# Kernel optimization log

Hardware: AMD Instinct MI355X
Metric: run time of the kernel (lower is better)

The kernel has to match this reference:

```python
import jax, jax.numpy as jnp
import numpy as np

N_NODES = 50000
N_EDGES = 800000
N_RELS = 16
D = 128


def _rgcn_layer(h, W, b, loop_w, gate_w, src, dst, rel, norm, apply_relu, n_nodes):
    # Transform all node features by every relation weight once: [R, N, D_out].
    # Equivalent to DGL bmm_maybe_select's per-edge W[rel] bmm, but avoids an
    # [E, D, D] gather of weights.
    h_all = jnp.einsum('nd,rde->rne', h, W)
    msg = h_all[rel, src]                                    # [E, D_out]
    msg = msg * norm                                         # edge norm scaling
    gate_logit = jnp.einsum('nd,rd->rn', h, gate_w[..., 0])  # [R, N]
    gate = jax.nn.sigmoid(gate_logit[rel, src])[:, None]     # [E, 1]
    msg = msg * gate
    agg = jax.ops.segment_sum(msg, dst, num_segments=n_nodes)  # fn.sum -> dst
    out = agg + b + h @ loop_w                               # bias + self loop
    if apply_relu:
        out = jax.nn.relu(out)
    return out  # dropout is identity in eval mode


def setup_inputs() -> dict:
    key = jax.random.key(0)
    ks = jax.random.split(key, 12)
    gain = float(np.sqrt(2.0))  # relu gain (xavier-ish scale; values arbitrary)
    def xav(k, shape):
        fan = shape[-2] + shape[-1]
        s = gain * np.sqrt(6.0 / fan)
        return jax.random.uniform(k, shape, jnp.float32, -s, s)
    return {
        'h': jax.random.normal(ks[0], (N_NODES, D), jnp.float32),
        'norm': jax.random.uniform(ks[1], (N_EDGES, 1), jnp.float32),
        'weight0': xav(ks[2], (N_RELS, D, D)),
        'bias0': jnp.zeros((D,), jnp.float32),
        'loop_w0': xav(ks[3], (D, D)),
        'gate_w0': xav(ks[4], (N_RELS, D, 1)),
        'weight1': xav(ks[5], (N_RELS, D, D)),
        'bias1': jnp.zeros((D,), jnp.float32),
        'loop_w1': xav(ks[6], (D, D)),
        'gate_w1': xav(ks[7], (N_RELS, D, 1)),
        'src': jax.random.randint(ks[8], (N_EDGES,), 0, N_NODES, jnp.int32),
        'dst': jax.random.randint(ks[9], (N_EDGES,), 0, N_NODES, jnp.int32),
        'rel_type': jax.random.randint(ks[10], (N_EDGES,), 0, N_RELS, jnp.int32),
    }


def reference(h, norm, weight0, bias0, loop_w0, gate_w0,
              weight1, bias1, loop_w1, gate_w1, src, dst, rel_type):
    n_nodes = h.shape[0]
    # Layer 0: activation=relu (idx < num_hidden_layers - 1)
    h = _rgcn_layer(h, weight0, bias0, loop_w0, gate_w0, src, dst, rel_type,
                    norm, True, n_nodes)
    # Layer 1: no activation
    h = _rgcn_layer(h, weight1, bias1, loop_w1, gate_w1, src, dst, rel_type,
                    norm, False, n_nodes)
    return h
```

## Files before the change

kernel.cpp:

```cpp
#include <hip/hip_runtime.h>
#include <hip/hip_bf16.h>
#include <stdint.h>

#define NN 50000
#define NE 800000
#define NR 16
#define NP (NN * NR)
#define NB1 ((NP + 255) / 256)
#define NTILES ((NN + 127) / 128)

typedef unsigned short u16;
typedef unsigned int u32;

typedef __bf16 bf16x8 __attribute__((ext_vector_type(8)));
typedef __bf16 bf16x2 __attribute__((ext_vector_type(2)));
typedef float f32x4 __attribute__((ext_vector_type(4)));

__device__ __forceinline__ u16 f2bf(float f) {
  u32 u = __float_as_uint(f);
  u = u + 0x7FFFu + ((u >> 16) & 1u);
  return (u16)(u >> 16);
}

__device__ __forceinline__ u32 pk2bf(float x, float y) {
#if __has_builtin(__builtin_amdgcn_cvt_pk_bf16_f32)
  bf16x2 r = __builtin_amdgcn_cvt_pk_bf16_f32(x, y);
  union { bf16x2 v; u32 u; } c;
  c.v = r;
  return c.u;
#else
  return (u32)f2bf(x) | ((u32)f2bf(y) << 16);
#endif
}

__device__ __forceinline__ float bflo(u32 w) { return __uint_as_float(w << 16); }
__device__ __forceinline__ float bfhi(u32 w) { return __uint_as_float(w & 0xFFFF0000u); }

__global__ void hist_kernel(const int* __restrict__ dst, const int* __restrict__ rel,
                            int* __restrict__ counts) {
  int e = blockIdx.x * 256 + threadIdx.x;
  if (e < NE) atomicAdd(&counts[dst[e] * NR + rel[e]], 1);
}

__global__ void scan_partial(const int* __restrict__ counts, int* __restrict__ bsum) {
  __shared__ int buf[256];
  int t = threadIdx.x;
  int i = blockIdx.x * 256 + t;
  int v = (i < NP) ? counts[i] : 0;
  buf[t] = v;
  __syncthreads();
  for (int off = 1; off < 256; off <<= 1) {
    int x = buf[t];
    int y = (t >= off) ? buf[t - off] : 0;
    __syncthreads();
    buf[t] = x + y;
    __syncthreads();
  }
  if (t == 255) bsum[blockIdx.x] = buf[255];
}

__global__ void scan_mid(const int* __restrict__ bsum, int* __restrict__ boff,
                         int* __restrict__ total_out) {
  __shared__ int buf[1024];
  int t = threadIdx.x;
  int v[4];
  int sum = 0;
#pragma unroll
  for (int i = 0; i < 4; ++i) {
    int idx = t * 4 + i;
    v[i] = (idx < NB1) ? bsum[idx] : 0;
    sum += v[i];
  }
  buf[t] = sum;
  __syncthreads();
  for (int off = 1; off < 1024; off <<= 1) {
    int x = buf[t];
    int y = (t >= off) ? buf[t - off] : 0;
    __syncthreads();
    buf[t] = x + y;
    __syncthreads();
  }
  int excl = buf[t] - sum;
#pragma unroll
  for (int i = 0; i < 4; ++i) {
    int idx = t * 4 + i;
    if (idx < NB1) { boff[idx] = excl; excl += v[i]; }
  }
  if (t == 1023) *total_out = buf[1023];
}

__global__ void scan_final(const int* __restrict__ counts, const int* __restrict__ boff,
                           int* __restrict__ starts, int* __restrict__ cursor) {
  __shared__ int buf[256];
  int t = threadIdx.x;
  int i = blockIdx.x * 256 + t;
  int v = (i < NP) ? counts[i] : 0;
  buf[t] = v;
  __syncthreads();
  for (int off = 1; off < 256; off <<= 1) {
    int x = buf[t];
    int y = (t >= off) ? buf[t - off] : 0;
    __syncthreads();
    buf[t] = x + y;
    __syncthreads();
  }
  int s = boff[blockIdx.x] + buf[t] - v;
  if (i < NP) {
    starts[i] = s;
    cursor[i] = s;
  }
}

__global__ void scatter_kernel(const int* __restrict__ src, const int* __restrict__ dst,
                               const int* __restrict__ rel, const float* __restrict__ norm,
                               int* __restrict__ cursor, u32* __restrict__ rowidx,
                               float* __restrict__ norm_s) {
  int e = blockIdx.x * 256 + threadIdx.x;
  if (e < NE) {
    int d = dst[e];
    int r = rel[e];
    int pos = atomicAdd(&cursor[d * NR + r], 1);
    rowidx[pos] = (u32)(r * NN + src[e]);
    norm_s[pos] = norm[e];
  }
}

__global__ void convert_wt(const float* __restrict__ w0, const float* __restrict__ lw0,
                           const float* __restrict__ w1, const float* __restrict__ lw1,
                           u16* __restrict__ Wt) {
  int m = blockIdx.y;
  int idx = blockIdx.x * 256 + threadIdx.x;
  int d = idx >> 7, k = idx & 127;
  const float* s;
  if (m < 16) s = w0 + (size_t)m * 16384;
  else if (m == 16) s = lw0;
  else if (m < 33) s = w1 + (size_t)(m - 17) * 16384;
  else s = lw1;
  Wt[(size_t)m * 16384 + idx] = f2bf(s[k * 128 + d]);
}

__global__ void hconv_kernel(const float* __restrict__ h, u16* __restrict__ hbf) {
  int i = blockIdx.x * 256 + threadIdx.x;
  float4 v = ((const float4*)h)[i];
  ushort4 u;
  u.x = f2bf(v.x); u.y = f2bf(v.y); u.z = f2bf(v.z); u.w = f2bf(v.w);
  ((ushort4*)hbf)[i] = u;
}

__global__ void gates_kernel(const u16* __restrict__ hbf, const float* __restrict__ gw,
                             float* __restrict__ gates) {
  __shared__ float hs[16 * 132];
  __shared__ float gws[16 * 132];
  int t = threadIdx.x;
  int n0 = blockIdx.x * 16;
#pragma unroll
  for (int i = 0; i < 2; ++i) {
    int f = t + 256 * i;
    int row = f >> 5, c4 = (f & 31) * 4;
    ushort4 u = *(const ushort4*)&hbf[(size_t)(n0 + row) * 128 + c4];
    hs[row * 132 + c4 + 0] = __uint_as_float((u32)u.x << 16);
    hs[row * 132 + c4 + 1] = __uint_as_float((u32)u.y << 16);
    hs[row * 132 + c4 + 2] = __uint_as_float((u32)u.z << 16);
    hs[row * 132 + c4 + 3] = __uint_as_float((u32)u.w << 16);
    *(float4*)&gws[row * 132 + c4] = *(const float4*)&gw[row * 128 + c4];
  }
  __syncthreads();
  int nl = t >> 4, r = t & 15;
  float s = 0.f;
#pragma unroll 8
  for (int k = 0; k < 128; ++k) s += hs[nl * 132 + k] * gws[r * 132 + k];
  gates[r * NN + n0 + nl] = 1.f / (1.f + __expf(-s));
}

__global__ void coef_kernel(const u32* __restrict__ rowidx,
                            const float* __restrict__ norm_s,
                            const float* __restrict__ gates, float* __restrict__ coef) {
  int e = blockIdx.x * 256 + threadIdx.x;
  if (e < NE) coef[e] = gates[rowidx[e]] * norm_s[e];
}

__global__ __launch_bounds__(256, 2)
void transform_kernel(const u16* __restrict__ hbf, const u16* __restrict__ Wtbase,
                      u16* __restrict__ th) {
  __shared__ u16 As[128 * 136];
  __shared__ u16 Ws[128 * 136];
  int t = threadIdx.x;
  int n0 = blockIdx.x * 128;
  int m = blockIdx.y;
  const u16* wmat = Wtbase + (size_t)m * 16384;
  int wave = t >> 6, lane = t & 63;
  int wd = (wave & 1) * 64, wn = (wave >> 1) * 64;
  int mrow = lane & 15, quad = lane >> 4;

#pragma unroll
  for (int i = 0; i < 8; ++i) {
    int u8i = t + 256 * i;
    int row = u8i >> 4, c8 = (u8i & 15) * 8;
    int n = n0 + row;
    int nc = n < NN ? n : NN - 1;
    *(uint4*)&Ws[row * 136 + c8] = *(const uint4*)&wmat[row * 128 + c8];
    *(uint4*)&As[row * 136 + c8] = *(const uint4*)&hbf[(size_t)nc * 128 + c8];
  }
  __syncthreads();

  f32x4 acc[4][4];
#pragma unroll
  for (int i = 0; i < 4; ++i)
#pragma unroll
    for (int j = 0; j < 4; ++j) acc[i][j] = (f32x4){0.f, 0.f, 0.f, 0.f};

#pragma unroll
  for (int kk = 0; kk < 4; ++kk) {
    int k0 = kk * 32 + quad * 8;
    bf16x8 fa[4], fb[4];
#pragma unroll
    for (int i2 = 0; i2 < 4; ++i2)
      fa[i2] = *(const bf16x8*)&Ws[(wd + i2 * 16 + mrow) * 136 + k0];
#pragma unroll
    for (int j2 = 0; j2 < 4; ++j2)
      fb[j2] = *(const bf16x8*)&As[(wn + j2 * 16 + mrow) * 136 + k0];
#pragma unroll
    for (int i2 = 0; i2 < 4; ++i2)
#pragma unroll
      for (int j2 = 0; j2 < 4; ++j2)
        acc[i2][j2] = __builtin_amdgcn_mfma_f32_16x16x32_bf16(fa[i2], fb[j2],
                                                              acc[i2][j2], 0, 0, 0);
  }

#pragma unroll
  for (int j = 0; j < 4; ++j) {
    int n = n0 + wn + j * 16 + mrow;
    if (n < NN) {
#pragma unroll
      for (int i = 0; i < 4; ++i) {
        int d0 = wd + i * 16 + quad * 4;
        uint2 st;
        st.x = pk2bf(acc[i][j][0], acc[i][j][1]);
        st.y = pk2bf(acc[i][j][2], acc[i][j][3]);
        *(uint2*)&th[((size_t)m * NN + n) * 128 + d0] = st;
      }
    }
  }
}

template <int LAYER>
__global__ __launch_bounds__(256)
void gatheradd_kernel(const u16* __restrict__ th, const u32* __restrict__ rowidx,
                      const float* __restrict__ coef, const int* __restrict__ starts,
                      const float* __restrict__ bias,
                      u16* __restrict__ hb_out, float* __restrict__ fout) {
  const u32* th32 = (const u32*)th;
  int wave = threadIdx.x >> 6;
  u32 lane = (u32)(threadIdx.x & 63);
  int v = blockIdx.x * 4 + wave;
  int s = starts[v * NR];
  int e = starts[v * NR + NR];
  float a0 = 0.f, a1 = 0.f;
  for (int j = s; j < e; j += 8) {
    u32 ri[8];
    float cf[8];
#pragma unroll
    for (int i = 0; i < 8; ++i) {
      int ii = (j + i < e) ? (j + i) : (e - 1);
      ri[i] = rowidx[ii];
      cf[i] = (j + i < e) ? coef[ii] : 0.f;
    }
    u32 w[8];
#pragma unroll
    for (int i = 0; i < 8; ++i) w[i] = th32[ri[i] * 64u + lane];
#pragma unroll
    for (int i = 0; i < 8; ++i) {
      a0 = fmaf(cf[i], bflo(w[i]), a0);
      a1 = fmaf(cf[i], bfhi(w[i]), a1);
    }
  }
  u32 ts = th32[((u32)(16 * NN) + (u32)v) * 64u + lane];
  float2 bv = *(const float2*)&bias[lane * 2u];
  a0 += bflo(ts) + bv.x;
  a1 += bfhi(ts) + bv.y;
  if (LAYER == 0) {
    a0 = fmaxf(a0, 0.f);
    a1 = fmaxf(a1, 0.f);
    ((u32*)hb_out)[(size_t)v * 64 + lane] = pk2bf(a0, a1);
  } else {
    *(float2*)&fout[(size_t)v * 128 + lane * 2u] = make_float2(a0, a1);
  }
}

extern "C" void kernel_launch(void* const* d_in, const int* in_sizes, int n_in,
                              void* d_out, int out_size, void* d_ws, size_t ws_size,
                              hipStream_t stream) {
  const float* h0   = (const float*)d_in[0];
  const float* norm = (const float*)d_in[1];
  const float* w0   = (const float*)d_in[2];
  const float* b0   = (const float*)d_in[3];
  const float* lw0  = (const float*)d_in[4];
  const float* gw0  = (const float*)d_in[5];
  const float* w1   = (const float*)d_in[6];
  const float* b1   = (const float*)d_in[7];
  const float* lw1  = (const float*)d_in[8];
  const float* gw1  = (const float*)d_in[9];
  const int*   src  = (const int*)d_in[10];
  const int*   dst  = (const int*)d_in[11];
  const int*   rel  = (const int*)d_in[12];
  float* out = (float*)d_out;

  char* p = (char*)d_ws;
  auto alloc = [&](size_t bytes) -> void* {
    void* q = (void*)p;
    p += (bytes + 255) & ~(size_t)255;
    return q;
  };
  u16*   Wt     = (u16*)alloc((size_t)34 * 16384 * 2);
  float* gates  = (float*)alloc((size_t)NR * NN * 4);
  u16*   hbf    = (u16*)alloc((size_t)NN * 128 * 2);
  int*   counts = (int*)alloc((size_t)NP * 4);
  int*   cursor = (int*)alloc((size_t)NP * 4);
  int*   starts = (int*)alloc((size_t)(NP + 1) * 4);
  int*   bsum   = (int*)alloc((size_t)NB1 * 4);
  int*   boff   = (int*)alloc((size_t)NB1 * 4);
  u32*   rowidx = (u32*)alloc((size_t)NE * 4);
  u16*   th     = (u16*)alloc((size_t)17 * NN * 128 * 2);
  float* norm_s = (float*)counts;
  float* coef   = (float*)cursor;

  hipMemsetAsync(counts, 0, (size_t)NP * 4, stream);
  hist_kernel<<<NE / 256, 256, 0, stream>>>(dst, rel, counts);
  scan_partial<<<NB1, 256, 0, stream>>>(counts, bsum);
  scan_mid<<<1, 1024, 0, stream>>>(bsum, boff, starts + NP);
  scan_final<<<NB1, 256, 0, stream>>>(counts, boff, starts, cursor);
  scatter_kernel<<<NE / 256, 256, 0, stream>>>(src, dst, rel, norm, cursor,
                                               rowidx, norm_s);
  convert_wt<<<dim3(64, 34), 256, 0, stream>>>(w0, lw0, w1, lw1, Wt);
  hconv_kernel<<<NN * 32 / 256, 256, 0, stream>>>(h0, hbf);

  gates_kernel<<<NN / 16, 256, 0, stream>>>(hbf, gw0, gates);
  coef_kernel<<<(NE + 255) / 256, 256, 0, stream>>>(rowidx, norm_s, gates, coef);
  transform_kernel<<<dim3(NTILES, 17), 256, 0, stream>>>(hbf, Wt, th);
  gatheradd_kernel<0><<<NN / 4, 256, 0, stream>>>(th, rowidx, coef, starts, b0,
                                                  hbf, nullptr);

  gates_kernel<<<NN / 16, 256, 0, stream>>>(hbf, gw1, gates);
  coef_kernel<<<(NE + 255) / 256, 256, 0, stream>>>(rowidx, norm_s, gates, coef);
  transform_kernel<<<dim3(NTILES, 17), 256, 0, stream>>>(hbf, Wt + (size_t)17 * 16384,
                                                         th);
  gatheradd_kernel<1><<<NN / 4, 256, 0, stream>>>(th, rowidx, coef, starts, b1,
                                                  nullptr, out);
}
```

Baseline: 483.3 us.

## Restructure transform GEMM: XCD-aware tile order, direct weight loads, 512 threads

The transform kernel moves from a 2D grid to a 1D grid with an XCD-aware remap, so that all 17 relation matrices for one node tile run on the same XCD and can share the h tile in L2. It drops the shared-memory weight tile, reading weight fragments straight from global/L2 with double-buffered prefetch. It also moves to 512 threads per block with a smaller per-wave output tile, which halves LDS use and raises occupancy. Separately, the gather-add loop is unrolled to 16 edges per iteration to keep more loads in flight, at the cost of extra registers and more wasted loads on short segments.

Result: slower. 586.0 us (+21.3%).

```diff
diff --git a/kernel.cpp b/kernel.cpp
--- a/kernel.cpp
+++ b/kernel.cpp
@@ -8,6 +8,7 @@
 #define NP (NN * NR)
 #define NB1 ((NP + 255) / 256)
 #define NTILES ((NN + 127) / 128)
+#define NWG_T (NTILES * 17)
 
 typedef unsigned short u16;
 typedef unsigned int u32;
@@ -179,68 +180,88 @@
   if (e < NE) coef[e] = gates[rowidx[e]] * norm_s[e];
 }
 
-__global__ __launch_bounds__(256, 2)
+__global__ __launch_bounds__(512, 4)
 void transform_kernel(const u16* __restrict__ hbf, const u16* __restrict__ Wtbase,
                       u16* __restrict__ th) {
   __shared__ u16 As[128 * 136];
-  __shared__ u16 Ws[128 * 136];
-  int t = threadIdx.x;
-  int n0 = blockIdx.x * 128;
-  int m = blockIdx.y;
+  int orig = blockIdx.x;
+  int qq = NWG_T / 8, rr = NWG_T % 8;
+  int xcd = orig & 7, idx = orig >> 3;
+  int wgid = (xcd < rr ? xcd * (qq + 1) : rr * (qq + 1) + (xcd - rr) * qq) + idx;
+  int tile = wgid / 17, m = wgid % 17;
+  int n0 = tile * 128;
   const u16* wmat = Wtbase + (size_t)m * 16384;
+
+  int t = threadIdx.x;
   int wave = t >> 6, lane = t & 63;
-  int wd = (wave & 1) * 64, wn = (wave >> 1) * 64;
+  int wd = (wave & 1) * 64;
+  int wn = (wave >> 1) * 32;
   int mrow = lane & 15, quad = lane >> 4;
 
 #pragma unroll
-  for (int i = 0; i < 8; ++i) {
-    int u8i = t + 256 * i;
+  for (int i = 0; i < 4; ++i) {
+    int u8i = t + 512 * i;
     int row = u8i >> 4, c8 = (u8i & 15) * 8;
     int n = n0 + row;
     int nc = n < NN ? n : NN - 1;
-    *(uint4*)&Ws[row * 136 + c8] = *(const uint4*)&wmat[row * 128 + c8];
     *(uint4*)&As[row * 136 + c8] = *(const uint4*)&hbf[(size_t)nc * 128 + c8];
   }
   __syncthreads();
 
-  f32x4 acc[4][4];
+  f32x4 acc[4][2];
 #pragma unroll
   for (int i = 0; i < 4; ++i)
 #pragma unroll
-    for (int j = 0; j < 4; ++j) acc[i][j] = (f32x4){0.f, 0.f, 0.f, 0.f};
-
-#pragma unroll
-  for (int kk = 0; kk < 4; ++kk) {
-    int k0 = kk * 32 + quad * 8;
-    bf16x8 fa[4], fb[4];
-#pragma unroll
-    for (int i2 = 0; i2 < 4; ++i2)
-      fa[i2] = *(const bf16x8*)&Ws[(wd + i2 * 16 + mrow) * 136 + k0];
-#pragma unroll
-    for (int j2 = 0; j2 < 4; ++j2)
-      fb[j2] = *(const bf16x8*)&As[(wn + j2 * 16 + mrow) * 136 + k0];
-#pragma unroll
-    for (int i2 = 0; i2 < 4; ++i2)
-#pragma unroll
-      for (int j2 = 0; j2 < 4; ++j2)
-        acc[i2][j2] = __builtin_amdgcn_mfma_f32_16x16x32_bf16(fa[i2], fb[j2],
-                                                              acc[i2][j2], 0, 0, 0);
-  }
-
-#pragma unroll
-  for (int j = 0; j < 4; ++j) {
-    int n = n0 + wn + j * 16 + mrow;
+    for (int j = 0; j < 2; ++j) acc[i][j] = (f32x4){0.f, 0.f, 0.f, 0.f};
+
+  bf16x8 faA[4], faB[4];
+
+#define LDFA(F, KK)                                                           \
+  _Pragma("unroll")                                                           \
+  for (int i2 = 0; i2 < 4; ++i2)                                              \
+    F[i2] = *(const bf16x8*)&wmat[(wd + i2 * 16 + mrow) * 128 +               \
+                                  (KK) * 32 + quad * 8];
+
+#define DOK(F, KK)                                                            \
+  {                                                                           \
+    int k0 = (KK) * 32 + quad * 8;                                            \
+    bf16x8 fb[2];                                                             \
+    _Pragma("unroll")                                                         \
+    for (int j2 = 0; j2 < 2; ++j2)                                            \
+      fb[j2] = *(const bf16x8*)&As[(wn + j2 * 16 + mrow) * 136 + k0];         \
+    _Pragma("unroll")                                                         \
+    for (int i2 = 0; i2 < 4; ++i2)                                            \
+      _Pragma("unroll")                                                       \
+      for (int j2 = 0; j2 < 2; ++j2)                                          \
+        acc[i2][j2] = __builtin_amdgcn_mfma_f32_16x16x32_bf16(                \
+            F[i2], fb[j2], acc[i2][j2], 0, 0, 0);                             \
+  }
+
+  LDFA(faA, 0)
+  LDFA(faB, 1)
+  DOK(faA, 0)
+  LDFA(faA, 2)
+  DOK(faB, 1)
+  LDFA(faB, 3)
+  DOK(faA, 2)
+  DOK(faB, 3)
+
+#pragma unroll
+  for (int j2 = 0; j2 < 2; ++j2) {
+    int n = n0 + wn + j2 * 16 + mrow;
     if (n < NN) {
 #pragma unroll
-      for (int i = 0; i < 4; ++i) {
-        int d0 = wd + i * 16 + quad * 4;
+      for (int i2 = 0; i2 < 4; ++i2) {
+        int d0 = wd + i2 * 16 + quad * 4;
         uint2 st;
-        st.x = pk2bf(acc[i][j][0], acc[i][j][1]);
-        st.y = pk2bf(acc[i][j][2], acc[i][j][3]);
+        st.x = pk2bf(acc[i2][j2][0], acc[i2][j2][1]);
+        st.y = pk2bf(acc[i2][j2][2], acc[i2][j2][3]);
         *(uint2*)&th[((size_t)m * NN + n) * 128 + d0] = st;
       }
     }
   }
+#undef LDFA
+#undef DOK
 }
 
 template <int LAYER>
@@ -256,20 +277,20 @@
   int s = starts[v * NR];
   int e = starts[v * NR + NR];
   float a0 = 0.f, a1 = 0.f;
-  for (int j = s; j < e; j += 8) {
-    u32 ri[8];
-    float cf[8];
-#pragma unroll
-    for (int i = 0; i < 8; ++i) {
+  for (int j = s; j < e; j += 16) {
+    u32 ri[16];
+    float cf[16];
+#pragma unroll
+    for (int i = 0; i < 16; ++i) {
       int ii = (j + i < e) ? (j + i) : (e - 1);
       ri[i] = rowidx[ii];
       cf[i] = (j + i < e) ? coef[ii] : 0.f;
     }
-    u32 w[8];
-#pragma unroll
-    for (int i = 0; i < 8; ++i) w[i] = th32[ri[i] * 64u + lane];
-#pragma unroll
-    for (int i = 0; i < 8; ++i) {
+    u32 w[16];
+#pragma unroll
+    for (int i = 0; i < 16; ++i) w[i] = th32[ri[i] * 64u + lane];
+#pragma unroll
+    for (int i = 0; i < 16; ++i) {
       a0 = fmaf(cf[i], bflo(w[i]), a0);
       a1 = fmaf(cf[i], bfhi(w[i]), a1);
     }
@@ -336,14 +357,13 @@
 
   gates_kernel<<<NN / 16, 256, 0, stream>>>(hbf, gw0, gates);
   coef_kernel<<<(NE + 255) / 256, 256, 0, stream>>>(rowidx, norm_s, gates, coef);
-  transform_kernel<<<dim3(NTILES, 17), 256, 0, stream>>>(hbf, Wt, th);
+  transform_kernel<<<NWG_T, 512, 0, stream>>>(hbf, Wt, th);
   gatheradd_kernel<0><<<NN / 4, 256, 0, stream>>>(th, rowidx, coef, starts, b0,
                                                   hbf, nullptr);
 
   gates_kernel<<<NN / 16, 256, 0, stream>>>(hbf, gw1, gates);
   coef_kernel<<<(NE + 255) / 256, 256, 0, stream>>>(rowidx, norm_s, gates, coef);
-  transform_kernel<<<dim3(NTILES, 17), 256, 0, stream>>>(hbf, Wt + (size_t)17 * 16384,
-                                                         th);
+  transform_kernel<<<NWG_T, 512, 0, stream>>>(hbf, Wt + (size_t)17 * 16384, th);
   gatheradd_kernel<1><<<NN / 4, 256, 0, stream>>>(th, rowidx, coef, starts, b1,
                                                   nullptr, out);
 }
```
